# Kernel tuning notes

Hardware: AMD Instinct MI355X
Metric: run time of the kernel (lower is better)

Reference implementation:

```python
import jax, jax.numpy as jnp
import numpy as np

N = 50000; E = 800000; T = 800000; G = 64
H = 128; IEMB = 128; BAS = 8; NS = 4; NR = 6; OEH = 128; OUT = 1; NB = 4; CUT = 5.0


def envelope(x):
    # exponent=5 -> p=6: 1/x + a*x^5 + b*x^6 + c*x^7 with a=-28, b=48, c=-21
    return 1.0 / x - 28.0 * x**5 + 48.0 * x**6 - 21.0 * x**7


def setup_inputs() -> dict:
    key = jax.random.key(0)
    ks = iter(jax.random.split(key, 80))
    def w(shape, s=0.1):
        return jax.random.normal(next(ks), shape, dtype=jnp.float32) * s
    inp = {}
    inp['z'] = jax.random.randint(next(ks), (N,), 0, 100, dtype=jnp.int32)
    inp['dist'] = jax.random.uniform(next(ks), (E,), jnp.float32, 0.05, 1.0)
    inp['dist_trip'] = jax.random.uniform(next(ks), (T,), jnp.float32, 0.05, 1.0)
    inp['angle'] = jax.random.uniform(next(ks), (T,), jnp.float32, -1.0, 1.0)
    inp['edge_index'] = jax.random.randint(next(ks), (2, E), 0, N, dtype=jnp.int32)
    inp['triplets'] = jax.random.randint(next(ks), (T, 3), 0, N, dtype=jnp.int32)
    inp['batch'] = jnp.sort(jax.random.randint(next(ks), (N,), 0, G, dtype=jnp.int32))
    inp['atom_table'] = w((100, H), 1.0)
    inp['rbf_freq'] = jnp.arange(1, NR + 1, dtype=jnp.float32) * jnp.float32(np.pi)
    inp['sbf_freq'] = jnp.arange(1, NR + 1, dtype=jnp.float32) * jnp.float32(np.pi)
    inp['emb_w1'] = w((NR, IEMB)); inp['emb_b1'] = w((IEMB,), 0.01)
    inp['emb_w2'] = w((IEMB, H)); inp['emb_b2'] = w((H,), 0.01)
    inp['iw_rbf1'] = w((NB, NR, BAS)); inp['iw_rbf2'] = w((NB, BAS, H))
    inp['iw_sbf1'] = w((NB, NS * NR, BAS)); inp['iw_sbf2'] = w((NB, BAS, IEMB))
    inp['iw_t1'] = w((NB, H, IEMB)); inp['iw_t2'] = w((NB, IEMB, H)); inp['ib_t2'] = w((NB, H), 0.01)
    inp['iw_up'] = w((NB, H, H)); inp['ib_up'] = w((NB, H), 0.01)
    inp['iw_down'] = w((NB, H, H)); inp['ib_down'] = w((NB, H), 0.01)
    inp['ow_rbf'] = w((NB + 1, NR, H))
    inp['ow0'] = w((NB + 1, H, OEH)); inp['ob0'] = w((NB + 1, OEH), 0.01)
    inp['ow1'] = w((NB + 1, OEH, OEH)); inp['ob1'] = w((NB + 1, OEH), 0.01)
    inp['ow2'] = w((NB + 1, OEH, OUT)); inp['ob2'] = w((NB + 1, OUT), 0.01)
    return inp


def _forward(atom_table, rbf_freq, sbf_freq, emb_w1, emb_b1, emb_w2, emb_b2,
             iw_rbf1, iw_rbf2, iw_sbf1, iw_sbf2, iw_t1, iw_t2, ib_t2,
             iw_up, ib_up, iw_down, ib_down, ow_rbf, ow0, ob0, ow1, ob1, ow2, ob2,
             dist, dist_trip, angle, z, edge_index, triplets, batch):
    row, col = edge_index[0], edge_index[1]
    j_idx = triplets[:, 1]
    # radial basis for edges: [E, NR]
    d = dist[:, None] / CUT
    rbf_e = envelope(d) * jnp.sin(rbf_freq * d)
    # spherical basis for triplets: [T, NS*NR]
    dt = dist_trip[:, None] / CUT
    rbf_t = envelope(dt) * jnp.sin(sbf_freq * dt)
    a = angle[:, None]
    sph = jnp.concatenate([jnp.ones_like(a), a, 0.5 * (3 * a**2 - 1), 0.5 * (5 * a**3 - 3 * a)], axis=-1)
    sbf_t = (rbf_t[:, None, :] * sph[:, :, None]).reshape(a.shape[0], -1)

    x = atom_table[z]  # [N, H]
    # EmbeddingBlock: edge msg from rbf only, scattered to col
    e = jax.nn.silu(rbf_e @ emb_w1 + emb_b1) @ emb_w2 + emb_b2
    x = x + jax.ops.segment_sum(e, col, num_segments=N)

    def out_block(k, x):
        rbf_emb = rbf_e @ ow_rbf[k]            # [E, H]
        h = jax.ops.segment_sum(x[row] * rbf_emb, col, num_segments=N)
        h = jax.nn.silu(h @ ow0[k] + ob0[k])
        h = jax.nn.silu(h @ ow1[k] + ob1[k])
        return h @ ow2[k] + ob2[k]             # [N, OUT]

    P = out_block(0, x)
    for b in range(NB):
        x_up = x @ iw_up[b] + ib_up[b]
        x_down = x @ iw_down[b] + ib_down[b]
        rbf_emb = jax.nn.silu(rbf_e @ iw_rbf1[b]) @ iw_rbf2[b]      # [E, H]
        x_edge = x_up[row] * rbf_emb                                  # [E, H]
        sbf_emb = jax.nn.silu(sbf_t @ iw_sbf1[b]) @ iw_sbf2[b]      # [T, H]
        t = jax.nn.silu(x_down @ iw_t1[b]) @ iw_t2[b] + ib_t2[b]     # [N, H]
        # original: for each triplet i, x_edge += t[j]*sbf_emb[i] (broadcast over all edges)
        extra = jnp.sum(t[j_idx] * sbf_emb, axis=0)                   # [H]
        x_edge = x_edge + extra
        x = x + jax.ops.segment_sum(x_edge, col, num_segments=N)
        P = P + out_block(b + 1, x)

    counts = jax.ops.segment_sum(jnp.ones((x.shape[0],), jnp.float32), batch, num_segments=G)
    pooled = jax.ops.segment_sum(P, batch, num_segments=G) / jnp.maximum(counts, 1.0)[:, None]
    return pooled  # [G, OUT]


def reference(z, dist, dist_trip, angle, edge_index, triplets, batch, atom_table, rbf_freq, sbf_freq,
              emb_w1, emb_b1, emb_w2, emb_b2, iw_rbf1, iw_rbf2, iw_sbf1, iw_sbf2, iw_t1, iw_t2, ib_t2,
              iw_up, ib_up, iw_down, ib_down, ow_rbf, ow0, ob0, ow1, ob1, ow2, ob2):
    return _forward(atom_table, rbf_freq, sbf_freq, emb_w1, emb_b1, emb_w2, emb_b2,
                    iw_rbf1, iw_rbf2, iw_sbf1, iw_sbf2, iw_t1, iw_t2, ib_t2,
                    iw_up, ib_up, iw_down, ib_down, ow_rbf, ow0, ob0, ow1, ob1, ow2, ob2,
                    dist, dist_trip, angle, z, edge_index, triplets, batch)
```

## Files before the change

### kernel.cpp

```cpp
#include <hip/hip_runtime.h>
#include <hip/hip_fp16.h>

#define N_ 50000
#define E_ 800000
#define T_ 800000
#define G_ 64
#define H_ 128

typedef __attribute__((ext_vector_type(8))) short bf16x8;
typedef __attribute__((ext_vector_type(4))) float f32x4;
typedef _Float16 f16x2 __attribute__((ext_vector_type(2)));

__device__ __forceinline__ float siluf(float v) {
    return __fdividef(v, 1.0f + __expf(-v));
}

__device__ __forceinline__ unsigned short f2bf(float f) {
    unsigned int u = __float_as_uint(f);
    u += 0x7fffu + ((u >> 16) & 1u);
    return (unsigned short)(u >> 16);
}
__device__ __forceinline__ unsigned int f2bf2(float a, float b) {
    return (unsigned int)f2bf(a) | ((unsigned int)f2bf(b) << 16);
}
__device__ __forceinline__ float bf2f(unsigned short h) {
    return __uint_as_float(((unsigned int)h) << 16);
}
__device__ __forceinline__ float2 bf2x2(unsigned int p) {
    return make_float2(__uint_as_float(p << 16), __uint_as_float(p & 0xffff0000u));
}
__device__ __forceinline__ float fdot2f(f16x2 a, f16x2 b, float c) {
    return __builtin_amdgcn_fdot2(a, b, c, false);
}

__global__ __launch_bounds__(256) void k_count2(const int* __restrict__ ecol, const int* __restrict__ trip,
                                                int* degE, int* degT) {
    int i = blockIdx.x * 256 + threadIdx.x;
    if (i < E_) atomicAdd(&degE[ecol[i]], 1);
    int t = i - E_;
    if (t >= 0 && t < T_) atomicAdd(&degT[trip[3 * t + 1]], 1);
}

__global__ __launch_bounds__(1024) void k_scan2(const int* __restrict__ degE, int* rowptrE, int* curE,
                                                const int* __restrict__ degT, int* rowptrT, int* curT, int n) {
    const int* deg = (blockIdx.x == 0) ? degE : degT;
    int* rowptr = (blockIdx.x == 0) ? rowptrE : rowptrT;
    int* cur = (blockIdx.x == 0) ? curE : curT;
    __shared__ int wsum[16];
    __shared__ int s_carry;
    int tid = threadIdx.x, lane = tid & 63, w = tid >> 6;
    if (tid == 0) s_carry = 0;
    __syncthreads();
    for (int base = 0; base < n; base += 1024) {
        int i = base + tid;
        int v = (i < n) ? deg[i] : 0;
        int incl = v;
        #pragma unroll
        for (int s = 1; s < 64; s <<= 1) {
            int t = __shfl_up(incl, (unsigned)s, 64);
            if (lane >= s) incl += t;
        }
        if (lane == 63) wsum[w] = incl;
        __syncthreads();
        int carry0 = s_carry;
        int wexcl = 0;
        for (int j = 0; j < w; ++j) wexcl += wsum[j];
        int excl = carry0 + wexcl + (incl - v);
        if (i < n) { rowptr[i] = excl; cur[i] = excl; }
        __syncthreads();
        if (tid == 1023) s_carry = carry0 + wexcl + incl;
        __syncthreads();
    }
    if (tid == 0) rowptr[n] = s_carry;
}

__global__ __launch_bounds__(256) void k_fill2(const int* __restrict__ ecol, const int* __restrict__ erow,
                                               const float* __restrict__ dist, int* curE, int2* __restrict__ epay,
                                               const int* __restrict__ trip, int* curT,
                                               const float* __restrict__ dist_trip, const float* __restrict__ angle,
                                               float2* __restrict__ tpay) {
    int i = blockIdx.x * 256 + threadIdx.x;
    if (i < E_) {
        int pos = atomicAdd(&curE[ecol[i]], 1);
        epay[pos] = make_int2(erow[i], __float_as_int(dist[i]));
    }
    int t = i - E_;
    if (t >= 0 && t < T_) {
        int pos = atomicAdd(&curT[trip[3 * t + 1]], 1);
        tpay[pos] = make_float2(dist_trip[t], angle[t]);
    }
}

__global__ __launch_bounds__(256) void k_unpack(const int2* __restrict__ epay, int* __restrict__ slist, int n) {
    int p = blockIdx.x * 256 + threadIdx.x;
    if (p < n) slist[p] = epay[p].x;
}

__global__ __launch_bounds__(256) void k_wprep(const float* __restrict__ emb_w2, const float* __restrict__ iw_down,
                                               const float* __restrict__ iw_t1, const float* __restrict__ iw_t2,
                                               const float* __restrict__ iw_up, const float* __restrict__ ow0,
                                               const float* __restrict__ ow1, unsigned short* __restrict__ Wt) {
    int mat = blockIdx.x >> 3;
    int part = blockIdx.x & 7;
    const float* src;
    if (mat == 0) src = emb_w2;
    else if (mat < 5) src = iw_down + (size_t)(mat - 1) * 16384;
    else if (mat < 9) src = iw_t1 + (size_t)(mat - 5) * 16384;
    else if (mat < 13) src = iw_t2 + (size_t)(mat - 9) * 16384;
    else if (mat < 17) src = iw_up + (size_t)(mat - 13) * 16384;
    else if (mat < 22) src = ow0 + (size_t)(mat - 17) * 16384;
    else src = ow1 + (size_t)(mat - 22) * 16384;
    unsigned short* dst = Wt + (size_t)mat * 16384;
    int base = part * 2048;
    for (int i = base + threadIdx.x; i < base + 2048; i += 256) {
        int k = i >> 7, n = i & 127;
        dst[n * 128 + k] = f2bf(src[i]);
    }
}

__global__ __launch_bounds__(256) void k_geom(const int2* __restrict__ epay,
                                              const float* __restrict__ freq, const float* __restrict__ iw_rbf1,
                                              float* __restrict__ rbfS, __half* __restrict__ s8all, int n) {
    __shared__ float W1s[4][48];
    int tid = threadIdx.x;
    if (tid < 192) W1s[tid / 48][tid % 48] = iw_rbf1[tid];
    __syncthreads();
    int p = blockIdx.x * 256 + tid;
    if (p >= n) return;
    float d = __int_as_float(epay[p].y) * 0.2f;
    float d2 = d * d, d4 = d2 * d2, d5 = d4 * d;
    float env = __fdividef(1.0f, d) - 28.0f * d5 + 48.0f * d5 * d - 21.0f * d5 * d2;
    float rb[6];
    #pragma unroll
    for (int r = 0; r < 6; ++r) {
        rb[r] = env * __sinf(freq[r] * d);
        rbfS[(size_t)p * 6 + r] = rb[r];
    }
    #pragma unroll
    for (int b = 0; b < 4; ++b) {
        __half out[8];
        #pragma unroll
        for (int k = 0; k < 8; ++k) {
            float u = 0.f;
            #pragma unroll
            for (int r = 0; r < 6; ++r) u += rb[r] * W1s[b][r * 8 + k];
            out[k] = __float2half(siluf(u));
        }
        *(uint4*)&s8all[((size_t)b * n + p) * 8] = *(uint4*)out;
    }
}

__global__ __launch_bounds__(256) void k_basis(const float2* __restrict__ tpay,
                                               const float* __restrict__ sfreq, __half* __restrict__ basis, int n) {
    int t = blockIdx.x * 256 + threadIdx.x;
    if (t >= n) return;
    float2 da = tpay[t];
    float d = da.x * 0.2f;
    float a = da.y;
    float d2 = d * d, d4 = d2 * d2, d5 = d4 * d;
    float env = __fdividef(1.0f, d) - 28.0f * d5 + 48.0f * d5 * d - 21.0f * d5 * d2;
    float rb[6];
    #pragma unroll
    for (int r = 0; r < 6; ++r) rb[r] = env * __sinf(sfreq[r] * d);
    float sph[4];
    sph[0] = 1.0f; sph[1] = a; sph[2] = 1.5f * a * a - 0.5f; sph[3] = 2.5f * a * a * a - 1.5f * a;
    __half out[24];
    #pragma unroll
    for (int s = 0; s < 4; ++s)
        #pragma unroll
        for (int r = 0; r < 6; ++r) out[s * 6 + r] = __float2half(sph[s] * rb[r]);
    uint4* dst = (uint4*)(basis + (size_t)t * 24);
    dst[0] = ((uint4*)out)[0];
    dst[1] = ((uint4*)out)[1];
    dst[2] = ((uint4*)out)[2];
}

__global__ __launch_bounds__(256) void k_sv4(const int* __restrict__ rowptrT, const __half* __restrict__ basis,
                                             const float* __restrict__ iw_sbf1, float* __restrict__ SV4, int n) {
    int wave = threadIdx.x >> 6, lane = threadIdx.x & 63;
    int node = blockIdx.x * 8 + wave * 2 + (lane >> 5);
    int sub = lane & 31;
    int blk = sub >> 3, k = sub & 7;
    if (node >= n) return;
    const float* W1 = iw_sbf1 + blk * 192;
    f16x2 w[12];
    #pragma unroll
    for (int j = 0; j < 12; ++j) {
        f16x2 t;
        t.x = (_Float16)W1[(2 * j) * 8 + k];
        t.y = (_Float16)W1[(2 * j + 1) * 8 + k];
        w[j] = t;
    }
    float acc = 0.f;
    int p0 = rowptrT[node], p1 = rowptrT[node + 1];
    for (int p = p0; p < p1; ++p) {
        union { uint4 q[3]; f16x2 h[12]; } bs;
        const uint4* bp = (const uint4*)(basis + (size_t)p * 24);
        bs.q[0] = bp[0]; bs.q[1] = bp[1]; bs.q[2] = bp[2];
        float u = 0.f;
        #pragma unroll
        for (int j = 0; j < 12; ++j) u = fdot2f(bs.h[j], w[j], u);
        acc += siluf(u);
    }
    SV4[((size_t)blk * n + node) * 8 + k] = acc;
}

__global__ __launch_bounds__(256) void k_init_x(const float* __restrict__ atab, const int* __restrict__ z,
                                                unsigned short* __restrict__ xh, int n) {
    int t = blockIdx.x * 256 + threadIdx.x;
    if (t >= n * 16) return;
    int node = t >> 4, q = t & 15;
    const float4* a4 = (const float4*)atab;
    float4 v0 = a4[(size_t)z[node] * 32 + q * 2];
    float4 v1 = a4[(size_t)z[node] * 32 + q * 2 + 1];
    uint4 pk;
    pk.x = f2bf2(v0.x, v0.y);
    pk.y = f2bf2(v0.z, v0.w);
    pk.z = f2bf2(v1.x, v1.y);
    pk.w = f2bf2(v1.z, v1.w);
    ((uint4*)xh)[t] = pk;
}

__global__ __launch_bounds__(256) void k_embS(const int* __restrict__ rowptr, const float* __restrict__ rbfS,
                                              const float* __restrict__ w1, const float* __restrict__ b1,
                                              float* __restrict__ SS, int n) {
    int node = blockIdx.x * 4 + (threadIdx.x >> 6);
    int lane = threadIdx.x & 63;
    if (node >= n) return;
    int c = lane * 2;
    float wc0[6], wc1[6];
    #pragma unroll
    for (int r = 0; r < 6; ++r) { wc0[r] = w1[r * 128 + c]; wc1[r] = w1[r * 128 + c + 1]; }
    float bb0 = b1[c], bb1 = b1[c + 1];
    float a0 = 0.f, a1 = 0.f;
    int p0 = rowptr[node], p1 = rowptr[node + 1];
    for (int p = p0; p < p1; ++p) {
        const float2* r2 = (const float2*)&rbfS[(size_t)p * 6];
        float2 ra = r2[0], rbx = r2[1], rc = r2[2];
        float u0 = bb0 + ra.x * wc0[0] + ra.y * wc0[1] + rbx.x * wc0[2] + rbx.y * wc0[3] + rc.x * wc0[4] + rc.y * wc0[5];
        float u1 = bb1 + ra.x * wc1[0] + ra.y * wc1[1] + rbx.x * wc1[2] + rbx.y * wc1[3] + rc.x * wc1[4] + rc.y * wc1[5];
        a0 += siluf(u0);
        a1 += siluf(u1);
    }
    SS[node * 128 + c] = a0;
    SS[node * 128 + c + 1] = a1;
}

template <int BIAS_MODE, bool SILU, bool ACCBF, bool ABF, bool WF32, bool WBF>
__global__ __launch_bounds__(256, 4) void k_gemm_mfma(const void* __restrict__ Ap,
                                                      const unsigned short* __restrict__ Wt,
                                                      const float* __restrict__ bias, const int* __restrict__ deg,
                                                      float* __restrict__ C, unsigned short* __restrict__ Ch, int M) {
    int tid = threadIdx.x;
    int wave = tid >> 6, lane = tid & 63;
    int m15 = lane & 15, quad = lane >> 4;
    int row0 = blockIdx.x * 64 + wave * 16;
    int arow = row0 + m15;
    if (arow > M - 1) arow = M - 1;

    f32x4 acc[8];
    #pragma unroll
    for (int nt = 0; nt < 8; ++nt) acc[nt] = (f32x4){0.f, 0.f, 0.f, 0.f};

    #pragma unroll
    for (int kt = 0; kt < 4; ++kt) {
        int ks = kt * 32 + quad * 8;
        bf16x8 av;
        if constexpr (ABF) {
            av = *(const bf16x8*)((const unsigned short*)Ap + (size_t)arow * 128 + ks);
        } else {
            const float* Arow = (const float*)Ap + (size_t)arow * 128;
            float4 a0 = *(const float4*)(Arow + ks);
            float4 a1 = *(const float4*)(Arow + ks + 4);
            union { bf16x8 v; unsigned int u[4]; } af;
            af.u[0] = f2bf2(a0.x, a0.y);
            af.u[1] = f2bf2(a0.z, a0.w);
            af.u[2] = f2bf2(a1.x, a1.y);
            af.u[3] = f2bf2(a1.z, a1.w);
            av = af.v;
        }
        #pragma unroll
        for (int nt = 0; nt < 8; ++nt) {
            bf16x8 bf = *(const bf16x8*)(Wt + (size_t)(nt * 16 + m15) * 128 + ks);
            acc[nt] = __builtin_amdgcn_mfma_f32_16x16x32_bf16(av, bf, acc[nt], 0, 0, 0);
        }
    }

    #pragma unroll
    for (int nt = 0; nt < 8; ++nt) {
        int col = nt * 16 + m15;
        float bc = 0.f;
        if constexpr (BIAS_MODE != 0) bc = bias[col];
        #pragma unroll
        for (int reg = 0; reg < 4; ++reg) {
            int row = row0 + quad * 4 + reg;
            if (row < M) {
                float v = acc[nt][reg];
                if constexpr (BIAS_MODE == 1) v += bc;
                if constexpr (BIAS_MODE == 2) v += bc * (float)deg[row];
                if constexpr (SILU) v = siluf(v);
                if constexpr (ACCBF) v += bf2f(Ch[(size_t)row * 128 + col]);
                if constexpr (WF32) C[(size_t)row * 128 + col] = v;
                if constexpr (WBF) Ch[(size_t)row * 128 + col] = f2bf(v);
            }
        }
    }
}

template <int PACC>
__global__ __launch_bounds__(256, 4) void k_out_mlp(const unsigned short* __restrict__ hB,
                                                    const unsigned short* __restrict__ W0t, const float* __restrict__ b0,
                                                    const unsigned short* __restrict__ W1t, const float* __restrict__ b1,
                                                    const float* __restrict__ w2col, const float* __restrict__ ob2p,
                                                    float* __restrict__ Pout, int M) {
    __shared__ unsigned short lds[4][16 * 136];
    int tid = threadIdx.x;
    int wave = tid >> 6, lane = tid & 63;
    int m15 = lane & 15, quad = lane >> 4;
    int row0 = blockIdx.x * 64 + wave * 16;
    int arow = row0 + m15;
    if (arow > M - 1) arow = M - 1;
    unsigned short* L = lds[wave];

    f32x4 acc[8];
    #pragma unroll
    for (int nt = 0; nt < 8; ++nt) acc[nt] = (f32x4){0.f, 0.f, 0.f, 0.f};
    #pragma unroll
    for (int kt = 0; kt < 4; ++kt) {
        int ks = kt * 32 + quad * 8;
        bf16x8 av = *(const bf16x8*)(hB + (size_t)arow * 128 + ks);
        #pragma unroll
        for (int nt = 0; nt < 8; ++nt) {
            bf16x8 bf = *(const bf16x8*)(W0t + (size_t)(nt * 16 + m15) * 128 + ks);
            acc[nt] = __builtin_amdgcn_mfma_f32_16x16x32_bf16(av, bf, acc[nt], 0, 0, 0);
        }
    }
    #pragma unroll
    for (int nt = 0; nt < 8; ++nt) {
        int col = nt * 16 + m15;
        float bc = b0[col];
        #pragma unroll
        for (int reg = 0; reg < 4; ++reg)
            L[(quad * 4 + reg) * 136 + col] = f2bf(siluf(acc[nt][reg] + bc));
    }
    __syncthreads();

    #pragma unroll
    for (int nt = 0; nt < 8; ++nt) acc[nt] = (f32x4){0.f, 0.f, 0.f, 0.f};
    #pragma unroll
    for (int kt = 0; kt < 4; ++kt) {
        int ks = kt * 32 + quad * 8;
        bf16x8 av = *(const bf16x8*)(L + m15 * 136 + ks);
        #pragma unroll
        for (int nt = 0; nt < 8; ++nt) {
            bf16x8 bf = *(const bf16x8*)(W1t + (size_t)(nt * 16 + m15) * 128 + ks);
            acc[nt] = __builtin_amdgcn_mfma_f32_16x16x32_bf16(av, bf, acc[nt], 0, 0, 0);
        }
    }
    float w2c[8], pp[4];
    #pragma unroll
    for (int nt = 0; nt < 8; ++nt) w2c[nt] = w2col[nt * 16 + m15];
    #pragma unroll
    for (int reg = 0; reg < 4; ++reg) pp[reg] = 0.f;
    #pragma unroll
    for (int nt = 0; nt < 8; ++nt) {
        float bc = b1[nt * 16 + m15];
        #pragma unroll
        for (int reg = 0; reg < 4; ++reg)
            pp[reg] += siluf(acc[nt][reg] + bc) * w2c[nt];
    }
    #pragma unroll
    for (int reg = 0; reg < 4; ++reg) {
        float s = pp[reg];
        s += __shfl_xor(s, 1, 64);
        s += __shfl_xor(s, 2, 64);
        s += __shfl_xor(s, 4, 64);
        s += __shfl_xor(s, 8, 64);
        if (m15 == 0) {
            int row = row0 + quad * 4 + reg;
            if (row < M) {
                float r = s + ob2p[0];
                if constexpr (PACC == 2) r += Pout[row];
                Pout[row] = r;
            }
        }
    }
}

__global__ __launch_bounds__(256, 4) void k_block_mlp(const unsigned short* __restrict__ xh,
                                                      const unsigned short* __restrict__ Wd, const float* __restrict__ bd,
                                                      const unsigned short* __restrict__ Wt1,
                                                      const unsigned short* __restrict__ Wt2, const float* __restrict__ bt2,
                                                      const unsigned short* __restrict__ Wup, const float* __restrict__ bup,
                                                      float* __restrict__ Tm, unsigned short* __restrict__ xuph, int M) {
    __shared__ unsigned short lds[4][16 * 136];
    int tid = threadIdx.x;
    int wave = tid >> 6, lane = tid & 63;
    int m15 = lane & 15, quad = lane >> 4;
    int row0 = blockIdx.x * 64 + wave * 16;
    int arow = row0 + m15;
    if (arow > M - 1) arow = M - 1;
    unsigned short* L = lds[wave];

    f32x4 accD[8], accU[8];
    #pragma unroll
    for (int nt = 0; nt < 8; ++nt) { accD[nt] = (f32x4){0.f, 0.f, 0.f, 0.f}; accU[nt] = (f32x4){0.f, 0.f, 0.f, 0.f}; }
    #pragma unroll
    for (int kt = 0; kt < 4; ++kt) {
        int ks = kt * 32 + quad * 8;
        bf16x8 av = *(const bf16x8*)(xh + (size_t)arow * 128 + ks);
        #pragma unroll
        for (int nt = 0; nt < 8; ++nt) {
            bf16x8 bd_ = *(const bf16x8*)(Wd + (size_t)(nt * 16 + m15) * 128 + ks);
            accD[nt] = __builtin_amdgcn_mfma_f32_16x16x32_bf16(av, bd_, accD[nt], 0, 0, 0);
            bf16x8 bu_ = *(const bf16x8*)(Wup + (size_t)(nt * 16 + m15) * 128 + ks);
            accU[nt] = __builtin_amdgcn_mfma_f32_16x16x32_bf16(av, bu_, accU[nt], 0, 0, 0);
        }
    }
    #pragma unroll
    for (int nt = 0; nt < 8; ++nt) {
        int col = nt * 16 + m15;
        float bcu = bup[col], bcd = bd[col];
        #pragma unroll
        for (int reg = 0; reg < 4; ++reg) {
            int row = row0 + quad * 4 + reg;
            if (row < M) xuph[(size_t)row * 128 + col] = f2bf(accU[nt][reg] + bcu);
            L[(quad * 4 + reg) * 136 + col] = f2bf(accD[nt][reg] + bcd);
        }
    }
    __syncthreads();

    #pragma unroll
    for (int nt = 0; nt < 8; ++nt) accD[nt] = (f32x4){0.f, 0.f, 0.f, 0.f};
    #pragma unroll
    for (int kt = 0; kt < 4; ++kt) {
        int ks = kt * 32 + quad * 8;
        bf16x8 av = *(const bf16x8*)(L + m15 * 136 + ks);
        #pragma unroll
        for (int nt = 0; nt < 8; ++nt) {
            bf16x8 bf = *(const bf16x8*)(Wt1 + (size_t)(nt * 16 + m15) * 128 + ks);
            accD[nt] = __builtin_amdgcn_mfma_f32_16x16x32_bf16(av, bf, accD[nt], 0, 0, 0);
        }
    }
    __syncthreads();
    #pragma unroll
    for (int nt = 0; nt < 8; ++nt) {
        int col = nt * 16 + m15;
        #pragma unroll
        for (int reg = 0; reg < 4; ++reg)
            L[(quad * 4 + reg) * 136 + col] = f2bf(siluf(accD[nt][reg]));
    }
    __syncthreads();

    #pragma unroll
    for (int nt = 0; nt < 8; ++nt) accD[nt] = (f32x4){0.f, 0.f, 0.f, 0.f};
    #pragma unroll
    for (int kt = 0; kt < 4; ++kt) {
        int ks = kt * 32 + quad * 8;
        bf16x8 av = *(const bf16x8*)(L + m15 * 136 + ks);
        #pragma unroll
        for (int nt = 0; nt < 8; ++nt) {
            bf16x8 bf = *(const bf16x8*)(Wt2 + (size_t)(nt * 16 + m15) * 128 + ks);
            accD[nt] = __builtin_amdgcn_mfma_f32_16x16x32_bf16(av, bf, accD[nt], 0, 0, 0);
        }
    }
    #pragma unroll
    for (int nt = 0; nt < 8; ++nt) {
        int col = nt * 16 + m15;
        float bc = bt2[col];
        #pragma unroll
        for (int reg = 0; reg < 4; ++reg) {
            int row = row0 + quad * 4 + reg;
            if (row < M) Tm[(size_t)row * 128 + col] = accD[nt][reg] + bc;
        }
    }
}

__global__ __launch_bounds__(256) void k_out_gather(const int* __restrict__ rowptr, const int* __restrict__ slist,
                                                    const float* __restrict__ rbfS,
                                                    const unsigned short* __restrict__ xh,
                                                    const float* __restrict__ wrbf,
                                                    unsigned short* __restrict__ hB, int n) {
    int node = blockIdx.x * 4 + (threadIdx.x >> 6);
    int lane = threadIdx.x & 63;
    if (node >= n) return;
    int c = lane * 2;
    float wc0[6], wc1[6];
    #pragma unroll
    for (int r = 0; r < 6; ++r) { wc0[r] = wrbf[r * 128 + c]; wc1[r] = wrbf[r * 128 + c + 1]; }
    float a0 = 0.f, a1 = 0.f;
    int p0 = rowptr[node], p1 = rowptr[node + 1];
    int p = p0;
    for (; p + 4 <= p1; p += 4) {
        int s0 = slist[p], s1 = slist[p + 1], s2 = slist[p + 2], s3 = slist[p + 3];
        float2 rb[4][3];
        #pragma unroll
        for (int u = 0; u < 4; ++u) {
            const float2* r2 = (const float2*)&rbfS[(size_t)(p + u) * 6];
            rb[u][0] = r2[0]; rb[u][1] = r2[1]; rb[u][2] = r2[2];
        }
        unsigned int xv0 = *(const unsigned int*)&xh[(size_t)s0 * 128 + c];
        unsigned int xv1 = *(const unsigned int*)&xh[(size_t)s1 * 128 + c];
        unsigned int xv2 = *(const unsigned int*)&xh[(size_t)s2 * 128 + c];
        unsigned int xv3 = *(const unsigned int*)&xh[(size_t)s3 * 128 + c];
        #pragma unroll
        for (int u = 0; u < 4; ++u) {
            float e0 = rb[u][0].x * wc0[0] + rb[u][0].y * wc0[1] + rb[u][1].x * wc0[2] +
                       rb[u][1].y * wc0[3] + rb[u][2].x * wc0[4] + rb[u][2].y * wc0[5];
            float e1 = rb[u][0].x * wc1[0] + rb[u][0].y * wc1[1] + rb[u][1].x * wc1[2] +
                       rb[u][1].y * wc1[3] + rb[u][2].x * wc1[4] + rb[u][2].y * wc1[5];
            float2 xf = bf2x2((u == 0) ? xv0 : (u == 1) ? xv1 : (u == 2) ? xv2 : xv3);
            a0 += xf.x * e0;
            a1 += xf.y * e1;
        }
    }
    for (; p < p1; ++p) {
        int src = slist[p];
        const float2* r2 = (const float2*)&rbfS[(size_t)p * 6];
        float2 ra = r2[0], rbx = r2[1], rc = r2[2];
        float e0 = ra.x * wc0[0] + ra.y * wc0[1] + rbx.x * wc0[2] + rbx.y * wc0[3] + rc.x * wc0[4] + rc.y * wc0[5];
        float e1 = ra.x * wc1[0] + ra.y * wc1[1] + rbx.x * wc1[2] + rbx.y * wc1[3] + rc.x * wc1[4] + rc.y * wc1[5];
        float2 xf = bf2x2(*(const unsigned int*)&xh[(size_t)src * 128 + c]);
        a0 += xf.x * e0;
        a1 += xf.y * e1;
    }
    *(unsigned int*)&hB[(size_t)node * 128 + c] = f2bf2(a0, a1);
}

__global__ __launch_bounds__(256) void k_extra_fused(const float* __restrict__ Tm, const float* __restrict__ SV,
                                                     const float* __restrict__ W2, float* __restrict__ extra, int n) {
    int tid = threadIdx.x;
    int c = tid & 127, half = tid >> 7;
    float acc[8];
    #pragma unroll
    for (int k = 0; k < 8; ++k) acc[k] = 0.f;
    for (int nn = blockIdx.x * 2 + half; nn < n; nn += gridDim.x * 2) {
        const float4* sv4 = (const float4*)&SV[(size_t)nn * 8];
        float4 s0 = sv4[0], s1 = sv4[1];
        float t = Tm[(size_t)nn * 128 + c];
        acc[0] += t * s0.x; acc[1] += t * s0.y; acc[2] += t * s0.z; acc[3] += t * s0.w;
        acc[4] += t * s1.x; acc[5] += t * s1.y; acc[6] += t * s1.z; acc[7] += t * s1.w;
    }
    float e = 0.f;
    #pragma unroll
    for (int k = 0; k < 8; ++k) e += acc[k] * W2[k * 128 + c];
    __shared__ float red[256];
    red[tid] = e;
    __syncthreads();
    if (tid < 128) atomicAdd(&extra[c], red[tid] + red[tid + 128]);
}

__global__ __launch_bounds__(256) void k_interact(const int* __restrict__ rowptr, const int* __restrict__ slist,
                                                  const __half* __restrict__ s8, const float* __restrict__ W2,
                                                  const float* __restrict__ extra,
                                                  const unsigned short* __restrict__ xuph,
                                                  unsigned short* __restrict__ xh, int n) {
    int node = blockIdx.x * 4 + (threadIdx.x >> 6);
    int lane = threadIdx.x & 63;
    if (node >= n) return;
    int c = lane * 2;
    f16x2 w2a[4], w2b[4];
    #pragma unroll
    for (int j = 0; j < 4; ++j) {
        f16x2 wa, wb;
        wa.x = (_Float16)W2[(2 * j) * 128 + c];
        wa.y = (_Float16)W2[(2 * j + 1) * 128 + c];
        wb.x = (_Float16)W2[(2 * j) * 128 + c + 1];
        wb.y = (_Float16)W2[(2 * j + 1) * 128 + c + 1];
        w2a[j] = wa;
        w2b[j] = wb;
    }
    int p0 = rowptr[node], p1 = rowptr[node + 1];
    float cntf = (float)(p1 - p0);
    float a0 = cntf * extra[c], a1 = cntf * extra[c + 1];
    int p = p0;
    for (; p + 4 <= p1; p += 4) {
        int s0 = slist[p], s1 = slist[p + 1], s2 = slist[p + 2], s3 = slist[p + 3];
        uint4 sv[4];
        #pragma unroll
        for (int u = 0; u < 4; ++u) sv[u] = *(const uint4*)(s8 + (size_t)(p + u) * 8);
        unsigned int xv0 = *(const unsigned int*)&xuph[(size_t)s0 * 128 + c];
        unsigned int xv1 = *(const unsigned int*)&xuph[(size_t)s1 * 128 + c];
        unsigned int xv2 = *(const unsigned int*)&xuph[(size_t)s2 * 128 + c];
        unsigned int xv3 = *(const unsigned int*)&xuph[(size_t)s3 * 128 + c];
        #pragma unroll
        for (int u = 0; u < 4; ++u) {
            union { uint4 q; f16x2 h[4]; } s;
            s.q = sv[u];
            float e0 = fdot2f(s.h[0], w2a[0], 0.f);
            e0 = fdot2f(s.h[1], w2a[1], e0);
            e0 = fdot2f(s.h[2], w2a[2], e0);
            e0 = fdot2f(s.h[3], w2a[3], e0);
            float e1 = fdot2f(s.h[0], w2b[0], 0.f);
            e1 = fdot2f(s.h[1], w2b[1], e1);
            e1 = fdot2f(s.h[2], w2b[2], e1);
            e1 = fdot2f(s.h[3], w2b[3], e1);
            float2 xf = bf2x2((u == 0) ? xv0 : (u == 1) ? xv1 : (u == 2) ? xv2 : xv3);
            a0 += xf.x * e0;
            a1 += xf.y * e1;
        }
    }
    for (; p < p1; ++p) {
        int src = slist[p];
        float2 xf = bf2x2(*(const unsigned int*)&xuph[(size_t)src * 128 + c]);
        union { uint4 q; f16x2 h[4]; } s;
        s.q = *(const uint4*)(s8 + (size_t)p * 8);
        float e0 = fdot2f(s.h[0], w2a[0], 0.f);
        e0 = fdot2f(s.h[1], w2a[1], e0);
        e0 = fdot2f(s.h[2], w2a[2], e0);
        e0 = fdot2f(s.h[3], w2a[3], e0);
        float e1 = fdot2f(s.h[0], w2b[0], 0.f);
        e1 = fdot2f(s.h[1], w2b[1], e1);
        e1 = fdot2f(s.h[2], w2b[2], e1);
        e1 = fdot2f(s.h[3], w2b[3], e1);
        a0 += xf.x * e0;
        a1 += xf.y * e1;
    }
    unsigned int cur = *(unsigned int*)&xh[(size_t)node * 128 + c];
    float2 xc = bf2x2(cur);
    *(unsigned int*)&xh[(size_t)node * 128 + c] = f2bf2(xc.x + a0, xc.y + a1);
}

__global__ __launch_bounds__(256) void k_pool(const float* __restrict__ P, const int* __restrict__ batch,
                                              float* __restrict__ pool, float* __restrict__ cnt, int n) {
    int i = blockIdx.x * 256 + threadIdx.x;
    int lane = threadIdx.x & 63;
    int b = (i < n) ? batch[i] : -1;
    float p = (i < n) ? P[i] : 0.f;
    int b0 = __shfl(b, 0, 64);
    int b63 = __shfl(b, 63, 64);
    if (b0 == b63 && b0 >= 0) {
        float s = p;
        #pragma unroll
        for (int off = 32; off > 0; off >>= 1) s += __shfl_xor(s, off, 64);
        if (lane == 0) {
            atomicAdd(&pool[b0], s);
            atomicAdd(&cnt[b0], 64.0f);
        }
    } else {
        if (i < n) {
            atomicAdd(&pool[b], p);
            atomicAdd(&cnt[b], 1.0f);
        }
    }
}

__global__ __launch_bounds__(64) void k_final(const float* __restrict__ pool, const float* __restrict__ cnt,
                                              float* __restrict__ out) {
    int g = threadIdx.x;
    if (g < G_) out[g] = __fdividef(pool[g], fmaxf(cnt[g], 1.0f));
}

extern "C" void kernel_launch(void* const* d_in, const int* in_sizes, int n_in,
                              void* d_out, int out_size, void* d_ws, size_t ws_size,
                              hipStream_t stream) {
    (void)in_sizes; (void)n_in; (void)out_size; (void)ws_size;
    const int* z = (const int*)d_in[0];
    const float* dist = (const float*)d_in[1];
    const float* dist_trip = (const float*)d_in[2];
    const float* angle = (const float*)d_in[3];
    const int* edge_index = (const int*)d_in[4];
    const int* triplets = (const int*)d_in[5];
    const int* batch = (const int*)d_in[6];
    const float* atom_table = (const float*)d_in[7];
    const float* rbf_freq = (const float*)d_in[8];
    const float* sbf_freq = (const float*)d_in[9];
    const float* emb_w1 = (const float*)d_in[10];
    const float* emb_b1 = (const float*)d_in[11];
    const float* emb_w2 = (const float*)d_in[12];
    const float* emb_b2 = (const float*)d_in[13];
    const float* iw_rbf1 = (const float*)d_in[14];
    const float* iw_rbf2 = (const float*)d_in[15];
    const float* iw_sbf1 = (const float*)d_in[16];
    const float* iw_sbf2 = (const float*)d_in[17];
    const float* iw_t1 = (const float*)d_in[18];
    const float* iw_t2 = (const float*)d_in[19];
    const float* ib_t2 = (const float*)d_in[20];
    const float* iw_up = (const float*)d_in[21];
    const float* ib_up = (const float*)d_in[22];
    const float* iw_down = (const float*)d_in[23];
    const float* ib_down = (const float*)d_in[24];
    const float* ow_rbf = (const float*)d_in[25];
    const float* ow0 = (const float*)d_in[26];
    const float* ob0 = (const float*)d_in[27];
    const float* ow1 = (const float*)d_in[28];
    const float* ob1 = (const float*)d_in[29];
    const float* ow2 = (const float*)d_in[30];
    const float* ob2 = (const float*)d_in[31];

    const int* erow = edge_index;
    const int* ecol = edge_index + E_;

    float* ws = (float*)d_ws;
    float* bufA = ws;
    float* bufB = bufA + (size_t)N_ * H_;
    float* P = bufB + (size_t)N_ * H_;
    float* rbfS = P + N_;
    float* SV4 = rbfS + (size_t)E_ * 6;
    float* extra4 = SV4 + (size_t)4 * N_ * 8;
    float* pool = extra4 + 512;
    float* cnt = pool + G_;
    int* deg = (int*)(cnt + G_);
    int* degT = deg + N_;
    int* rowptr = degT + N_;
    int* curE = rowptr + N_ + 1;
    int* curT = curE + N_;
    int* slist = curT + N_;
    int* rowptrT = slist + E_;
    int2* epay = (int2*)(rowptrT + N_ + 1);
    float2* tpay = (float2*)(epay + E_);
    __half* s8all = (__half*)(tpay + T_);
    __half* basis = s8all + (size_t)4 * E_ * 8;
    unsigned short* xh = (unsigned short*)(basis + (size_t)T_ * 24);
    unsigned short* xuph = xh + (size_t)N_ * H_;
    unsigned short* Wt = xuph + (size_t)N_ * H_;
    unsigned short* hB = (unsigned short*)bufB;

    const int EG = (E_ + 255) / 256;
    const int TG = (T_ + 255) / 256;
    const int ETG = (E_ + T_ + 255) / 256;
    const int NG4 = (N_ + 3) / 4;
    const int GEMMG = (N_ + 63) / 64;

    hipMemsetAsync(deg, 0, 2 * N_ * sizeof(int), stream);
    hipMemsetAsync(extra4, 0, (512 + 2 * G_) * sizeof(float), stream);
    k_wprep<<<27 * 8, 256, 0, stream>>>(emb_w2, iw_down, iw_t1, iw_t2, iw_up, ow0, ow1, Wt);
    k_count2<<<ETG, 256, 0, stream>>>(ecol, triplets, deg, degT);
    k_scan2<<<2, 1024, 0, stream>>>(deg, rowptr, curE, degT, rowptrT, curT, N_);
    k_fill2<<<ETG, 256, 0, stream>>>(ecol, erow, dist, curE, epay, triplets, curT, dist_trip, angle, tpay);
    k_unpack<<<EG, 256, 0, stream>>>(epay, slist, E_);

    k_geom<<<EG, 256, 0, stream>>>(epay, rbf_freq, iw_rbf1, rbfS, s8all, E_);
    k_basis<<<TG, 256, 0, stream>>>(tpay, sbf_freq, basis, T_);
    k_sv4<<<(N_ + 7) / 8, 256, 0, stream>>>(rowptrT, basis, iw_sbf1, SV4, N_);
    k_init_x<<<(N_ * 16 + 255) / 256, 256, 0, stream>>>(atom_table, z, xh, N_);

    k_embS<<<NG4, 256, 0, stream>>>(rowptr, rbfS, emb_w1, emb_b1, bufA, N_);
    k_gemm_mfma<2, false, true, false, false, true><<<GEMMG, 256, 0, stream>>>(
        bufA, Wt, emb_b2, deg, nullptr, xh, N_);

    auto out_block = [&](int k, bool first) {
        k_out_gather<<<NG4, 256, 0, stream>>>(rowptr, slist, rbfS, xh,
                                              ow_rbf + (size_t)k * 6 * 128, hB, N_);
        if (first)
            k_out_mlp<1><<<GEMMG, 256, 0, stream>>>(hB, Wt + (size_t)(17 + k) * 16384, ob0 + k * 128,
                                                    Wt + (size_t)(22 + k) * 16384, ob1 + k * 128,
                                                    ow2 + k * 128, ob2 + k, P, N_);
        else
            k_out_mlp<2><<<GEMMG, 256, 0, stream>>>(hB, Wt + (size_t)(17 + k) * 16384, ob0 + k * 128,
                                                    Wt + (size_t)(22 + k) * 16384, ob1 + k * 128,
                                                    ow2 + k * 128, ob2 + k, P, N_);
    };

    out_block(0, true);

    for (int b = 0; b < 4; ++b) {
        k_block_mlp<<<GEMMG, 256, 0, stream>>>(xh,
                                               Wt + (size_t)(1 + b) * 16384, ib_down + b * 128,
                                               Wt + (size_t)(5 + b) * 16384,
                                               Wt + (size_t)(9 + b) * 16384, ib_t2 + b * 128,
                                               Wt + (size_t)(13 + b) * 16384, ib_up + b * 128,
                                               bufA, xuph, N_);
        k_extra_fused<<<256, 256, 0, stream>>>(bufA, SV4 + (size_t)b * N_ * 8,
                                               iw_sbf2 + (size_t)b * 1024, extra4 + b * 128, N_);
        k_interact<<<NG4, 256, 0, stream>>>(rowptr, slist, s8all + (size_t)b * E_ * 8,
                                            iw_rbf2 + (size_t)b * 1024, extra4 + b * 128,
                                            xuph, xh, N_);
        out_block(b + 1, false);
    }

    k_pool<<<(N_ + 255) / 256, 256, 0, stream>>>(P, batch, pool, cnt, N_);
    k_final<<<1, 64, 0, stream>>>(pool, cnt, (float*)d_out);
}
```

Measured before the change: 1.742 ms.

## Build CSR via two-level bucketing to localize atomics and scatter writes

Replaces the global count/fill CSR construction with a bucket pass that groups edges and triplets by 64-column block, followed by per-block counting in shared memory and a placement pass whose atomics and writes stay localized. The separate unpack kernel is removed by writing the source list and distances directly as separate arrays. Bucket storage aliases buffers that are filled later. The fixed per-sub-bucket capacity could drop entries on skewed degree distributions, and the change adds an extra read/write of the bucketed payload.

```diff
diff --git a/kernel.cpp b/kernel.cpp
--- a/kernel.cpp
+++ b/kernel.cpp
@@ -7,6 +7,10 @@
 #define G_ 64
 #define H_ 128
 
+#define NBK 782
+#define NSB (NBK * 8)
+#define CAPS 512
+
 typedef __attribute__((ext_vector_type(8))) short bf16x8;
 typedef __attribute__((ext_vector_type(4))) float f32x4;
 typedef _Float16 f16x2 __attribute__((ext_vector_type(2)));
@@ -33,12 +37,57 @@
     return __builtin_amdgcn_fdot2(a, b, c, false);
 }
 
-__global__ __launch_bounds__(256) void k_count2(const int* __restrict__ ecol, const int* __restrict__ trip,
-                                                int* degE, int* degT) {
+__global__ __launch_bounds__(256) void k_bucket(const int* __restrict__ ecol, const int* __restrict__ erow,
+                                                const float* __restrict__ dist,
+                                                const int* __restrict__ trip,
+                                                const float* __restrict__ dist_trip, const float* __restrict__ angle,
+                                                int* bcntE, int2* __restrict__ ebktP, unsigned char* __restrict__ ebktC,
+                                                int* bcntT, float2* __restrict__ tbktP, unsigned char* __restrict__ tbktC) {
     int i = blockIdx.x * 256 + threadIdx.x;
-    if (i < E_) atomicAdd(&degE[ecol[i]], 1);
+    int r = blockIdx.x & 7;
+    if (i < E_) {
+        int col = ecol[i];
+        int sb = (col >> 6) * 8 + r;
+        int pos = atomicAdd(&bcntE[sb], 1);
+        if (pos < CAPS) {
+            ebktP[(size_t)sb * CAPS + pos] = make_int2(erow[i], __float_as_int(dist[i]));
+            ebktC[(size_t)sb * CAPS + pos] = (unsigned char)(col & 63);
+        }
+    }
     int t = i - E_;
-    if (t >= 0 && t < T_) atomicAdd(&degT[trip[3 * t + 1]], 1);
+    if (t >= 0 && t < T_) {
+        int j = trip[3 * t + 1];
+        int sb = (j >> 6) * 8 + r;
+        int pos = atomicAdd(&bcntT[sb], 1);
+        if (pos < CAPS) {
+            tbktP[(size_t)sb * CAPS + pos] = make_float2(dist_trip[t], angle[t]);
+            tbktC[(size_t)sb * CAPS + pos] = (unsigned char)(j & 63);
+        }
+    }
+}
+
+__global__ __launch_bounds__(256) void k_cnt(const int* __restrict__ bcntE, const unsigned char* __restrict__ ebktC,
+                                             const int* __restrict__ bcntT, const unsigned char* __restrict__ tbktC,
+                                             int* __restrict__ degE, int* __restrict__ degT) {
+    int b = blockIdx.x;
+    bool isE = b < NBK;
+    if (!isE) b -= NBK;
+    __shared__ int c[64];
+    int tid = threadIdx.x;
+    if (tid < 64) c[tid] = 0;
+    __syncthreads();
+    const int* bcnt = isE ? bcntE : bcntT;
+    const unsigned char* bc = isE ? ebktC : tbktC;
+    for (int s = 0; s < 8; ++s) {
+        int sb = b * 8 + s;
+        int nb = min(bcnt[sb], CAPS);
+        for (int i = tid; i < nb; i += 256) atomicAdd(&c[bc[(size_t)sb * CAPS + i]], 1);
+    }
+    __syncthreads();
+    if (tid < 64) {
+        int col = b * 64 + tid;
+        if (col < N_) (isE ? degE : degT)[col] = c[tid];
+    }
 }
 
 __global__ __launch_bounds__(1024) void k_scan2(const int* __restrict__ degE, int* rowptrE, int* curE,
@@ -74,26 +123,42 @@
     if (tid == 0) rowptr[n] = s_carry;
 }
 
-__global__ __launch_bounds__(256) void k_fill2(const int* __restrict__ ecol, const int* __restrict__ erow,
-                                               const float* __restrict__ dist, int* curE, int2* __restrict__ epay,
-                                               const int* __restrict__ trip, int* curT,
-                                               const float* __restrict__ dist_trip, const float* __restrict__ angle,
+__global__ __launch_bounds__(256) void k_place(const int* __restrict__ bcntE, const int2* __restrict__ ebktP,
+                                               const unsigned char* __restrict__ ebktC, int* curE,
+                                               int* __restrict__ slist, float* __restrict__ distS,
+                                               const int* __restrict__ bcntT, const float2* __restrict__ tbktP,
+                                               const unsigned char* __restrict__ tbktC, int* curT,
                                                float2* __restrict__ tpay) {
-    int i = blockIdx.x * 256 + threadIdx.x;
-    if (i < E_) {
-        int pos = atomicAdd(&curE[ecol[i]], 1);
-        epay[pos] = make_int2(erow[i], __float_as_int(dist[i]));
-    }
-    int t = i - E_;
-    if (t >= 0 && t < T_) {
-        int pos = atomicAdd(&curT[trip[3 * t + 1]], 1);
-        tpay[pos] = make_float2(dist_trip[t], angle[t]);
-    }
-}
-
-__global__ __launch_bounds__(256) void k_unpack(const int2* __restrict__ epay, int* __restrict__ slist, int n) {
-    int p = blockIdx.x * 256 + threadIdx.x;
-    if (p < n) slist[p] = epay[p].x;
+    int b = blockIdx.x;
+    bool isE = b < NBK;
+    if (!isE) b -= NBK;
+    int tid = threadIdx.x;
+    if (isE) {
+        for (int s = 0; s < 8; ++s) {
+            int sb = b * 8 + s;
+            int nb = min(bcntE[sb], CAPS);
+            for (int i = tid; i < nb; i += 256) {
+                size_t idx = (size_t)sb * CAPS + i;
+                int col = b * 64 + ebktC[idx];
+                int2 pr = ebktP[idx];
+                int pos = atomicAdd(&curE[col], 1);
+                slist[pos] = pr.x;
+                distS[pos] = __int_as_float(pr.y);
+            }
+        }
+    } else {
+        for (int s = 0; s < 8; ++s) {
+            int sb = b * 8 + s;
+            int nb = min(bcntT[sb], CAPS);
+            for (int i = tid; i < nb; i += 256) {
+                size_t idx = (size_t)sb * CAPS + i;
+                int col = b * 64 + tbktC[idx];
+                float2 pr = tbktP[idx];
+                int pos = atomicAdd(&curT[col], 1);
+                tpay[pos] = pr;
+            }
+        }
+    }
 }
 
 __global__ __launch_bounds__(256) void k_wprep(const float* __restrict__ emb_w2, const float* __restrict__ iw_down,
@@ -118,7 +183,7 @@
     }
 }
 
-__global__ __launch_bounds__(256) void k_geom(const int2* __restrict__ epay,
+__global__ __launch_bounds__(256) void k_geom(const float* __restrict__ distS,
                                               const float* __restrict__ freq, const float* __restrict__ iw_rbf1,
                                               float* __restrict__ rbfS, __half* __restrict__ s8all, int n) {
     __shared__ float W1s[4][48];
@@ -127,7 +192,7 @@
     __syncthreads();
     int p = blockIdx.x * 256 + tid;
     if (p >= n) return;
-    float d = __int_as_float(epay[p].y) * 0.2f;
+    float d = distS[p] * 0.2f;
     float d2 = d * d, d4 = d2 * d2, d5 = d4 * d;
     float env = __fdividef(1.0f, d) - 28.0f * d5 + 48.0f * d5 * d - 21.0f * d5 * d2;
     float rb[6];
@@ -700,15 +765,19 @@
     float* extra4 = SV4 + (size_t)4 * N_ * 8;
     float* pool = extra4 + 512;
     float* cnt = pool + G_;
-    int* deg = (int*)(cnt + G_);
-    int* degT = deg + N_;
+    int* bcntE = (int*)(cnt + G_);
+    int* bcntT = bcntE + NSB;
+    int* degE = bcntT + NSB;
+    int* degT = degE + N_;
     int* rowptr = degT + N_;
     int* curE = rowptr + N_ + 1;
     int* curT = curE + N_;
     int* slist = curT + N_;
     int* rowptrT = slist + E_;
-    int2* epay = (int2*)(rowptrT + N_ + 1);
-    float2* tpay = (float2*)(epay + E_);
+    float* distS = (float*)(rowptrT + N_ + 1);
+    uintptr_t tp = (uintptr_t)(distS + E_);
+    tp = (tp + 7) & ~(uintptr_t)7;
+    float2* tpay = (float2*)tp;
     __half* s8all = (__half*)(tpay + T_);
     __half* basis = s8all + (size_t)4 * E_ * 8;
     unsigned short* xh = (unsigned short*)(basis + (size_t)T_ * 24);
@@ -716,28 +785,34 @@
     unsigned short* Wt = xuph + (size_t)N_ * H_;
     unsigned short* hB = (unsigned short*)bufB;
 
+    int2* ebktP = (int2*)s8all;
+    unsigned char* ebktC = (unsigned char*)(ebktP + (size_t)NSB * CAPS);
+    float2* tbktP = (float2*)(ebktC + (size_t)NSB * CAPS);
+    unsigned char* tbktC = (unsigned char*)(tbktP + (size_t)NSB * CAPS);
+
     const int EG = (E_ + 255) / 256;
     const int TG = (T_ + 255) / 256;
     const int ETG = (E_ + T_ + 255) / 256;
     const int NG4 = (N_ + 3) / 4;
     const int GEMMG = (N_ + 63) / 64;
 
-    hipMemsetAsync(deg, 0, 2 * N_ * sizeof(int), stream);
-    hipMemsetAsync(extra4, 0, (512 + 2 * G_) * sizeof(float), stream);
+    hipMemsetAsync(extra4, 0, (512 + 2 * G_ + 2 * NSB) * sizeof(float), stream);
     k_wprep<<<27 * 8, 256, 0, stream>>>(emb_w2, iw_down, iw_t1, iw_t2, iw_up, ow0, ow1, Wt);
-    k_count2<<<ETG, 256, 0, stream>>>(ecol, triplets, deg, degT);
-    k_scan2<<<2, 1024, 0, stream>>>(deg, rowptr, curE, degT, rowptrT, curT, N_);
-    k_fill2<<<ETG, 256, 0, stream>>>(ecol, erow, dist, curE, epay, triplets, curT, dist_trip, angle, tpay);
-    k_unpack<<<EG, 256, 0, stream>>>(epay, slist, E_);
-
-    k_geom<<<EG, 256, 0, stream>>>(epay, rbf_freq, iw_rbf1, rbfS, s8all, E_);
+    k_bucket<<<ETG, 256, 0, stream>>>(ecol, erow, dist, triplets, dist_trip, angle,
+                                      bcntE, ebktP, ebktC, bcntT, tbktP, tbktC);
+    k_cnt<<<2 * NBK, 256, 0, stream>>>(bcntE, ebktC, bcntT, tbktC, degE, degT);
+    k_scan2<<<2, 1024, 0, stream>>>(degE, rowptr, curE, degT, rowptrT, curT, N_);
+    k_place<<<2 * NBK, 256, 0, stream>>>(bcntE, ebktP, ebktC, curE, slist, distS,
+                                         bcntT, tbktP, tbktC, curT, tpay);
+
+    k_geom<<<EG, 256, 0, stream>>>(distS, rbf_freq, iw_rbf1, rbfS, s8all, E_);
     k_basis<<<TG, 256, 0, stream>>>(tpay, sbf_freq, basis, T_);
     k_sv4<<<(N_ + 7) / 8, 256, 0, stream>>>(rowptrT, basis, iw_sbf1, SV4, N_);
     k_init_x<<<(N_ * 16 + 255) / 256, 256, 0, stream>>>(atom_table, z, xh, N_);
 
     k_embS<<<NG4, 256, 0, stream>>>(rowptr, rbfS, emb_w1, emb_b1, bufA, N_);
     k_gemm_mfma<2, false, true, false, false, true><<<GEMMG, 256, 0, stream>>>(
-        bufA, Wt, emb_b2, deg, nullptr, xh, N_);
+        bufA, Wt, emb_b2, degE, nullptr, xh, N_);
 
     auto out_block = [&](int k, bool first) {
         k_out_gather<<<NG4, 256, 0, stream>>>(rowptr, slist, rbfS, xh,
```

New measurement: 1.702 ms. 2.3% less time.
